# Kernel tuning notes

Hardware: AMD Instinct MI355X
Metric: run time of the kernel (lower is better)

## Reference

```python
import jax, jax.numpy as jnp
import numpy as np
import math

N = 32768
NUM_BATCH = 64
DIM_QK = 128
DIM_V = 256
M_FEATURES = 256
EPS_PHI = 1e-4
EPS_NORM = 1e-8


def _make_omega(nrows, ncols, rng):
    """Block-orthogonal random feature matrix, faithful to Attention._omega.
    Returns [ncols, nrows] (i.e. [dim_qk, m])."""
    nblocks = nrows // ncols
    blocks = []
    for _ in range(nblocks):
        q, _ = np.linalg.qr(rng.normal(size=(ncols, ncols)))
        blocks.append(q.T)
    missing = nrows - nblocks * ncols
    if missing > 0:
        q, _ = np.linalg.qr(rng.normal(size=(ncols, ncols)))
        blocks.append(q.T[:missing])
    norm = np.linalg.norm(rng.normal(size=(nrows, ncols)), axis=1, keepdims=True)
    return (norm * np.vstack(blocks)).T.astype(np.float32)


def setup_inputs() -> dict:
    key = jax.random.key(0)
    kq, kk, kv = jax.random.split(key, 3)
    Q = jax.random.normal(kq, (N, DIM_QK), dtype=jnp.float32)
    K = jax.random.normal(kk, (N, DIM_QK), dtype=jnp.float32)
    V = jax.random.normal(kv, (N, DIM_V), dtype=jnp.float32)
    # contiguous equal-size segments (64 molecules x 512 atoms)
    batch_seg = jnp.repeat(jnp.arange(NUM_BATCH, dtype=jnp.int32), N // NUM_BATCH)
    omega = jnp.asarray(_make_omega(M_FEATURES, DIM_QK, np.random.default_rng(0)))
    return {"Q": Q, "K": K, "V": V, "omega": omega,
            "num_batch": NUM_BATCH, "batch_seg": batch_seg}


def reference(Q, K, V, omega, num_batch, batch_seg):
    d = Q.shape[-1]
    m = omega.shape[-1]
    inv_sqrt_m = 1.0 / math.sqrt(m)

    def phi(X, is_query):
        U = (X / d ** 0.25) @ omega                       # [N, m]
        h = jnp.sum(X * X, axis=-1, keepdims=True) / (2.0 * d ** 0.5)
        if is_query:
            mx = jnp.max(U, axis=-1, keepdims=True)       # per-row max
        else:
            # per-segment max over all rows & features, gathered back per row
            seg_max = jax.ops.segment_max(jnp.max(U, axis=-1), batch_seg,
                                          num_segments=num_batch)
            mx = seg_max[batch_seg][:, None]
        return (jnp.exp(U - h - mx) + EPS_PHI) * inv_sqrt_m

    Qp = phi(Q, True)    # [N, m]
    Kp = phi(K, False)   # [N, m]

    # normalizer: Qp . (sum of Kp within segment)
    Ksum = jax.ops.segment_sum(Kp, batch_seg, num_segments=num_batch)  # [B, m]
    norm = jnp.sum(Qp * Ksum[batch_seg], axis=-1, keepdims=True) + EPS_NORM

    # Linear-attention equivalent of (mask * (Kp @ Qp^T))^T @ V:
    # out[i] = Qp[i] @ sum_{j in seg(i)} Kp[j] V[j]^T. Segments are
    # contiguous & equal-sized, so segment reductions become batched einsums.
    n_per = Q.shape[0] // num_batch
    Kpb = Kp.reshape(num_batch, n_per, m)
    Vb = V.reshape(num_batch, n_per, -1)
    KV = jnp.einsum('bnm,bnv->bmv', Kpb, Vb)              # [B, m, dv]
    Qpb = Qp.reshape(num_batch, n_per, m)
    out = jnp.einsum('bnm,bmv->bnv', Qpb, KV).reshape(Q.shape[0], -1)
    return out / norm
```

## Files before the change

### kernel.cpp

```cpp
#include <hip/hip_runtime.h>
#include <math.h>

#define NTOT 32768
#define NB   64
#define NPB  512
#define DQK  128
#define MF   256
#define DVV  256

#define QK_SCALE   0.29730177875068026f
#define INV_SQRT_M 0.0625f
#define EPS_PHI    1e-4f
#define EPS_NORM   1e-8f
#define EPS_ISM    (EPS_PHI * INV_SQRT_M)

typedef float f32x4  __attribute__((ext_vector_type(4)));
typedef short bf16x8 __attribute__((ext_vector_type(8)));
typedef unsigned short us4 __attribute__((ext_vector_type(4)));
typedef unsigned short us8 __attribute__((ext_vector_type(8)));

static __device__ __forceinline__ float red_max32(float v) {
    v = fmaxf(v, __shfl_xor(v, 1, 64));
    v = fmaxf(v, __shfl_xor(v, 2, 64));
    v = fmaxf(v, __shfl_xor(v, 4, 64));
    v = fmaxf(v, __shfl_xor(v, 8, 64));
    v = fmaxf(v, __shfl_xor(v, 16, 64));
    return v;
}
static __device__ __forceinline__ float red_sum16(float v) {
    v += __shfl_xor(v, 1, 64);
    v += __shfl_xor(v, 2, 64);
    v += __shfl_xor(v, 4, 64);
    v += __shfl_xor(v, 8, 64);
    return v;
}
static __device__ __forceinline__ float red_max16(float v) {
    v = fmaxf(v, __shfl_xor(v, 1, 64));
    v = fmaxf(v, __shfl_xor(v, 2, 64));
    v = fmaxf(v, __shfl_xor(v, 4, 64));
    v = fmaxf(v, __shfl_xor(v, 8, 64));
    return v;
}

static __device__ __forceinline__ void bfsplit(float x, unsigned short& h, unsigned short& l) {
    unsigned u = __float_as_uint(x);
    unsigned r = (u + 0x7fffu + ((u >> 16) & 1u)) & 0xffff0000u;
    h = (unsigned short)(r >> 16);
    float lo = x - __uint_as_float(r);
    unsigned v = __float_as_uint(lo);
    l = (unsigned short)((v + 0x7fffu + ((v >> 16) & 1u)) >> 16);
}

__global__ __launch_bounds__(256) void omsplit_kernel(
    const float* __restrict__ omega,
    unsigned short* __restrict__ OmFh, unsigned short* __restrict__ OmFl)
{
    const int k = blockIdx.x;
    const int m = threadIdx.x;
    unsigned short h, l;
    bfsplit(omega[k * MF + m], h, l);
    const int M16 = m >> 4, fr = m & 15;
    const int c = k >> 5, kk = k & 31;
    const int lane = fr + 16 * (kk >> 3);
    const size_t idx = ((size_t)(M16 * 4 + c) * 64 + lane) * 8 + (kk & 7);
    OmFh[idx] = h;
    OmFl[idx] = l;
}

template <bool IS_QUERY>
__global__ __launch_bounds__(256) void phi_kernel(
    const float* __restrict__ X,
    const unsigned short* __restrict__ OmFh, const unsigned short* __restrict__ OmFl,
    const float* __restrict__ Ksum,
    float* __restrict__ outF,
    unsigned short* __restrict__ outH, unsigned short* __restrict__ outL,
    float* __restrict__ aux)
{
    __shared__ __align__(16) float Xf[64][132];
    __shared__ float hS[64];
    __shared__ float mxW[4][64];
    __shared__ float npW[4][64];
    __shared__ float KsS[256];

    const int tid  = threadIdx.x;
    const int lane = tid & 63;
    const int w    = tid >> 6;
    const int fr   = lane & 15;
    const int k8   = (lane >> 4) * 8;
    const int rg   = (lane >> 4) * 4;
    const int row0 = blockIdx.x * 64;

    if (IS_QUERY) KsS[tid] = Ksum[(row0 >> 9) * MF + tid];

    float hp[8];
    {
        const float4* Xv = (const float4*)(X + (size_t)row0 * DQK);
        #pragma unroll
        for (int j = 0; j < 8; ++j) {
            int idx = tid + 256 * j;
            int r = idx >> 5, c4 = idx & 31;
            float4 v = Xv[idx];
            v.x *= QK_SCALE; v.y *= QK_SCALE; v.z *= QK_SCALE; v.w *= QK_SCALE;
            *(float4*)&Xf[r][c4 * 4] = v;
            hp[j] = v.x * v.x + v.y * v.y + v.z * v.z + v.w * v.w;
        }
    }
    __syncthreads();
    #pragma unroll
    for (int j = 0; j < 8; ++j) {
        hp[j] += __shfl_xor(hp[j], 1, 64);
        hp[j] += __shfl_xor(hp[j], 2, 64);
        hp[j] += __shfl_xor(hp[j], 4, 64);
        hp[j] += __shfl_xor(hp[j], 8, 64);
        hp[j] += __shfl_xor(hp[j], 16, 64);
    }
    if ((tid & 31) == 0) {
        #pragma unroll
        for (int j = 0; j < 8; ++j) hS[(tid >> 5) + 8 * j] = hp[j];
    }

    f32x4 acc[4][4] = {};
    #pragma unroll
    for (int c = 0; c < 4; ++c) {
        bf16x8 ah[4], al[4];
        #pragma unroll
        for (int t = 0; t < 4; ++t) {
            float a[8];
            *(float4*)&a[0] = *(const float4*)&Xf[t * 16 + fr][c * 32 + k8];
            *(float4*)&a[4] = *(const float4*)&Xf[t * 16 + fr][c * 32 + k8 + 4];
            unsigned short hh[8], ll[8];
            #pragma unroll
            for (int s = 0; s < 8; ++s) bfsplit(a[s], hh[s], ll[s]);
            ah[t] = *(bf16x8*)&hh[0];
            al[t] = *(bf16x8*)&ll[0];
        }
        #pragma unroll
        for (int u = 0; u < 4; ++u) {
            const size_t ob = ((size_t)((w * 4 + u) * 4 + c) * 64 + lane) * 8;
            bf16x8 bh = *(const bf16x8*)&OmFh[ob];
            bf16x8 bl = *(const bf16x8*)&OmFl[ob];
            #pragma unroll
            for (int t = 0; t < 4; ++t) {
                acc[t][u] = __builtin_amdgcn_mfma_f32_16x16x32_bf16(ah[t], bh, acc[t][u], 0, 0, 0);
                acc[t][u] = __builtin_amdgcn_mfma_f32_16x16x32_bf16(ah[t], bl, acc[t][u], 0, 0, 0);
                acc[t][u] = __builtin_amdgcn_mfma_f32_16x16x32_bf16(al[t], bh, acc[t][u], 0, 0, 0);
            }
        }
    }

    #pragma unroll
    for (int t = 0; t < 4; ++t) {
        #pragma unroll
        for (int g = 0; g < 4; ++g) {
            float m0 = fmaxf(fmaxf(acc[t][0][g], acc[t][1][g]),
                             fmaxf(acc[t][2][g], acc[t][3][g]));
            m0 = red_max16(m0);
            if (fr == 0) mxW[w][t * 16 + rg + g] = m0;
        }
    }
    __syncthreads();

    #pragma unroll
    for (int t = 0; t < 4; ++t) {
        #pragma unroll
        for (int g = 0; g < 4; ++g) {
            const int row  = t * 16 + rg + g;
            const int grow = row0 + row;
            const float mxa = fmaxf(fmaxf(mxW[0][row], mxW[1][row]),
                                    fmaxf(mxW[2][row], mxW[3][row]));
            const float hm = 0.5f * hS[row] + mxa;
            if (IS_QUERY) {
                float np = 0.f;
                #pragma unroll
                for (int u = 0; u < 4; ++u) {
                    const int col = w * 64 + u * 16 + fr;
                    const float q = (__expf(acc[t][u][g] - hm) + EPS_PHI) * INV_SQRT_M;
                    unsigned short qh, ql;
                    bfsplit(q, qh, ql);
                    outH[(size_t)grow * MF + col] = qh;
                    outL[(size_t)grow * MF + col] = ql;
                    np = fmaf(q, KsS[col], np);
                }
                np = red_sum16(np);
                if (fr == 0) npW[w][row] = np;
            } else {
                #pragma unroll
                for (int u = 0; u < 4; ++u)
                    outF[(size_t)grow * MF + w * 64 + u * 16 + fr] = __expf(acc[t][u][g] - hm);
                if (w == 0 && fr == 0) aux[grow] = mxa;
            }
        }
    }
    if (IS_QUERY) {
        __syncthreads();
        if (w == 0 && fr == 0) {
            #pragma unroll
            for (int t = 0; t < 4; ++t)
                #pragma unroll
                for (int g = 0; g < 4; ++g) {
                    const int row = t * 16 + rg + g;
                    aux[row0 + row] = npW[0][row] + npW[1][row] + npW[2][row] + npW[3][row];
                }
        }
    }
}

__global__ __launch_bounds__(256) void segsexp_kernel(
    const float* __restrict__ rmax, float* __restrict__ sexp)
{
    const int b = blockIdx.x, tid = threadIdx.x;
    const float r0 = rmax[b * NPB + tid];
    const float r1 = rmax[b * NPB + 256 + tid];
    float v = fmaxf(r0, r1);
    v = red_max32(v);
    v = fmaxf(v, __shfl_xor(v, 32, 64));
    __shared__ float red[4];
    if ((tid & 63) == 0) red[tid >> 6] = v;
    __syncthreads();
    const float smax = fmaxf(fmaxf(red[0], red[1]), fmaxf(red[2], red[3]));
    sexp[b * NPB + tid]       = __expf(r0 - smax);
    sexp[b * NPB + 256 + tid] = __expf(r1 - smax);
}

__global__ __launch_bounds__(256) void kv_kernel(
    const float* __restrict__ A, const float* __restrict__ V,
    const float* __restrict__ sexp,
    float* __restrict__ KV, float* __restrict__ P1,
    float* __restrict__ Ksum, float* __restrict__ KsumP)
{
    __shared__ __align__(16) float Af[32][132];
    __shared__ __align__(16) float Vf[32][132];
    __shared__ __align__(16) unsigned short KpH[128][40];
    __shared__ __align__(16) unsigned short KpL[128][40];
    __shared__ __align__(16) unsigned short VH[128][40];
    __shared__ __align__(16) unsigned short VL[128][40];

    const int tid  = threadIdx.x;
    const int lane = tid & 63;
    const int w    = tid >> 6;
    const int wr   = w >> 1;
    const int wc   = w & 1;
    const int fr   = lane & 15;
    const int k8   = (lane >> 4) * 8;
    const int rg   = (lane >> 4) * 4;

    const int vt = blockIdx.x, mt = blockIdx.y;
    const int b  = blockIdx.z >> 1, ch = blockIdx.z & 1;
    const int m0 = mt * 128, v0 = vt * 128;
    const size_t n0 = (size_t)b * NPB + ch * 256;

    const int ln  = tid >> 5;
    const int lm4 = tid & 31;
    const int tv  = tid >> 1;
    const int th  = tid & 1;

    f32x4 acc[4][4] = {};
    float4 ks4 = {0.f, 0.f, 0.f, 0.f};

    for (int c = 0; c < 8; ++c) {
        __syncthreads();
        #pragma unroll
        for (int j = 0; j < 4; ++j) {
            const size_t n = n0 + c * 32 + ln + 8 * j;
            float4 a  = *(const float4*)&A[n * MF + m0 + lm4 * 4];
            float4 vv = *(const float4*)&V[n * DVV + v0 + lm4 * 4];
            const float s2 = sexp[n] * INV_SQRT_M;
            float4 e;
            e.x = fmaf(a.x, s2, EPS_ISM);
            e.y = fmaf(a.y, s2, EPS_ISM);
            e.z = fmaf(a.z, s2, EPS_ISM);
            e.w = fmaf(a.w, s2, EPS_ISM);
            ks4.x += e.x; ks4.y += e.y; ks4.z += e.z; ks4.w += e.w;
            *(float4*)&Af[ln + 8 * j][lm4 * 4] = e;
            *(float4*)&Vf[ln + 8 * j][lm4 * 4] = vv;
        }
        __syncthreads();
        {
            unsigned short hh[16], ll[16];
            #pragma unroll
            for (int s = 0; s < 16; ++s)
                bfsplit(Af[th * 16 + s][tv], hh[s], ll[s]);
            *(us8*)&KpH[tv][th * 16]     = *(us8*)&hh[0];
            *(us8*)&KpH[tv][th * 16 + 8] = *(us8*)&hh[8];
            *(us8*)&KpL[tv][th * 16]     = *(us8*)&ll[0];
            *(us8*)&KpL[tv][th * 16 + 8] = *(us8*)&ll[8];
            #pragma unroll
            for (int s = 0; s < 16; ++s)
                bfsplit(Vf[th * 16 + s][tv], hh[s], ll[s]);
            *(us8*)&VH[tv][th * 16]     = *(us8*)&hh[0];
            *(us8*)&VH[tv][th * 16 + 8] = *(us8*)&hh[8];
            *(us8*)&VL[tv][th * 16]     = *(us8*)&ll[0];
            *(us8*)&VL[tv][th * 16 + 8] = *(us8*)&ll[8];
        }
        __syncthreads();
        bf16x8 ah[4], al[4];
        #pragma unroll
        for (int t = 0; t < 4; ++t) {
            ah[t] = *(const bf16x8*)&KpH[wr * 64 + t * 16 + fr][k8];
            al[t] = *(const bf16x8*)&KpL[wr * 64 + t * 16 + fr][k8];
        }
        #pragma unroll
        for (int u = 0; u < 4; ++u) {
            bf16x8 bh = *(const bf16x8*)&VH[wc * 64 + u * 16 + fr][k8];
            bf16x8 bl = *(const bf16x8*)&VL[wc * 64 + u * 16 + fr][k8];
            #pragma unroll
            for (int t = 0; t < 4; ++t) {
                acc[t][u] = __builtin_amdgcn_mfma_f32_16x16x32_bf16(ah[t], bh, acc[t][u], 0, 0, 0);
                acc[t][u] = __builtin_amdgcn_mfma_f32_16x16x32_bf16(ah[t], bl, acc[t][u], 0, 0, 0);
                acc[t][u] = __builtin_amdgcn_mfma_f32_16x16x32_bf16(al[t], bh, acc[t][u], 0, 0, 0);
            }
        }
    }

    float* __restrict__ dKV = ch ? P1 : KV;
    #pragma unroll
    for (int t = 0; t < 4; ++t) {
        #pragma unroll
        for (int g = 0; g < 4; ++g) {
            const int row = wr * 64 + t * 16 + rg + g;
            const size_t base = ((size_t)b * MF + m0 + row) * DVV + v0 + wc * 64;
            #pragma unroll
            for (int u = 0; u < 4; ++u)
                dKV[base + u * 16 + fr] = acc[t][u][g];
        }
    }

    if (vt == 0) {
        __syncthreads();
        float* scr = &Af[0][0];
        *(float4*)&scr[(ln * 32 + lm4) * 4] = ks4;
        __syncthreads();
        if (tid < 128) {
            float s = 0.f;
            #pragma unroll
            for (int g = 0; g < 8; ++g) s += scr[g * 128 + tid];
            (ch ? KsumP : Ksum)[b * MF + m0 + tid] = s;
        }
    }
}

__global__ __launch_bounds__(256) void kvreduce_kernel(
    float* __restrict__ KV, const float* __restrict__ P1,
    float* __restrict__ Ksum, const float* __restrict__ KsumP)
{
    const int idx = blockIdx.x * 256 + threadIdx.x;
    const int stride = gridDim.x * 256;
    const int TOT4 = NB * MF * DVV / 4;
    for (int i = idx; i < TOT4; i += stride) {
        float4 a = ((const float4*)KV)[i];
        float4 p = ((const float4*)P1)[i];
        a.x += p.x; a.y += p.y; a.z += p.z; a.w += p.w;
        ((float4*)KV)[i] = a;
    }
    const int KS4 = NB * MF / 4;
    for (int i = idx; i < KS4; i += stride) {
        float4 a = ((const float4*)Ksum)[i];
        float4 p = ((const float4*)KsumP)[i];
        a.x += p.x; a.y += p.y; a.z += p.z; a.w += p.w;
        ((float4*)Ksum)[i] = a;
    }
}

__global__ __launch_bounds__(256) void out_kernel(
    const unsigned short* __restrict__ QpH, const unsigned short* __restrict__ QpL,
    const float* __restrict__ KVm,
    const float* __restrict__ normv, float* __restrict__ out)
{
    __shared__ __align__(16) unsigned short Qh[128][40];
    __shared__ __align__(16) unsigned short Ql[128][40];
    __shared__ __align__(16) unsigned short Kh[128][40];
    __shared__ __align__(16) unsigned short Kl[128][40];
    __shared__ __align__(16) float Kf[32][132];
    __shared__ float nrmS[128];

    const int tid  = threadIdx.x;
    const int lane = tid & 63;
    const int w    = tid >> 6;
    const int wr   = w >> 1;
    const int wc   = w & 1;
    const int fr   = lane & 15;
    const int k8   = (lane >> 4) * 8;

    const int vt = blockIdx.x, rt = blockIdx.y, b = blockIdx.z;
    const int v0 = vt * 128;
    const int r0 = b * NPB + rt * 128;

    if (tid < 128) nrmS[tid] = normv[r0 + tid];

    const int qr  = tid >> 3;
    const int qm4 = tid & 7;
    const int km  = tid >> 5;
    const int kv4 = tid & 31;
    const int tv  = tid >> 1;
    const int th  = tid & 1;

    f32x4 acc[4][4] = {};

    for (int c = 0; c < 8; ++c) {
        const int mc = c * 32;
        __syncthreads();
        #pragma unroll
        for (int j = 0; j < 4; ++j) {
            const size_t qb = (size_t)(r0 + qr + 32 * j) * MF + mc + qm4 * 4;
            *(us4*)&Qh[qr + 32 * j][qm4 * 4] = *(const us4*)&QpH[qb];
            *(us4*)&Ql[qr + 32 * j][qm4 * 4] = *(const us4*)&QpL[qb];
            *(float4*)&Kf[km + 8 * j][kv4 * 4] =
                *(const float4*)&KVm[((size_t)b * MF + mc + km + 8 * j) * DVV + v0 + kv4 * 4];
        }
        __syncthreads();
        {
            unsigned short hh[16], ll[16];
            #pragma unroll
            for (int s = 0; s < 16; ++s)
                bfsplit(Kf[th * 16 + s][tv], hh[s], ll[s]);
            *(us8*)&Kh[tv][th * 16]     = *(us8*)&hh[0];
            *(us8*)&Kh[tv][th * 16 + 8] = *(us8*)&hh[8];
            *(us8*)&Kl[tv][th * 16]     = *(us8*)&ll[0];
            *(us8*)&Kl[tv][th * 16 + 8] = *(us8*)&ll[8];
        }
        __syncthreads();
        bf16x8 ah[4], al[4];
        #pragma unroll
        for (int t = 0; t < 4; ++t) {
            ah[t] = *(const bf16x8*)&Qh[wr * 64 + t * 16 + fr][k8];
            al[t] = *(const bf16x8*)&Ql[wr * 64 + t * 16 + fr][k8];
        }
        #pragma unroll
        for (int u = 0; u < 4; ++u) {
            bf16x8 bh = *(const bf16x8*)&Kh[wc * 64 + u * 16 + fr][k8];
            bf16x8 bl = *(const bf16x8*)&Kl[wc * 64 + u * 16 + fr][k8];
            #pragma unroll
            for (int t = 0; t < 4; ++t) {
                acc[t][u] = __builtin_amdgcn_mfma_f32_16x16x32_bf16(ah[t], bh, acc[t][u], 0, 0, 0);
                acc[t][u] = __builtin_amdgcn_mfma_f32_16x16x32_bf16(ah[t], bl, acc[t][u], 0, 0, 0);
                acc[t][u] = __builtin_amdgcn_mfma_f32_16x16x32_bf16(al[t], bh, acc[t][u], 0, 0, 0);
            }
        }
    }

    const int rg = (lane >> 4) * 4;
    #pragma unroll
    for (int t = 0; t < 4; ++t) {
        #pragma unroll
        for (int g = 0; g < 4; ++g) {
            const int row = wr * 64 + t * 16 + rg + g;
            const float inv = 1.0f / (nrmS[row] + EPS_NORM);
            const size_t base = (size_t)(r0 + row) * DVV + v0 + wc * 64;
            #pragma unroll
            for (int u = 0; u < 4; ++u)
                out[base + u * 16 + fr] = acc[t][u][g] * inv;
        }
    }
}

extern "C" void kernel_launch(void* const* d_in, const int* in_sizes, int n_in,
                              void* d_out, int out_size, void* d_ws, size_t ws_size,
                              hipStream_t stream)
{
    const float* Q     = (const float*)d_in[0];
    const float* K     = (const float*)d_in[1];
    const float* V     = (const float*)d_in[2];
    const float* omega = (const float*)d_in[3];
    float* out = (float*)d_out;

    float* ws    = (float*)d_ws;
    float* Qp    = ws;
    float* A     = Qp    + (size_t)NTOT * MF;
    float* KV    = A     + (size_t)NTOT * MF;
    float* Ksum  = KV    + (size_t)NB * MF * DVV;
    float* KsumP = Ksum  + (size_t)NB * MF;
    float* rmaxA = KsumP + (size_t)NB * MF;
    float* sexp  = rmaxA + NTOT;
    float* normv = sexp  + NTOT;
    unsigned short* OmFh = (unsigned short*)(normv + NTOT);
    unsigned short* OmFl = OmFh + (size_t)MF * DQK;

    float* P1 = Qp;
    unsigned short* QpH = (unsigned short*)Qp;
    unsigned short* QpL = QpH + (size_t)NTOT * MF;

    omsplit_kernel<<<DQK, 256, 0, stream>>>(omega, OmFh, OmFl);
    phi_kernel<false><<<NTOT / 64, 256, 0, stream>>>(K, OmFh, OmFl, (const float*)nullptr,
                                                     A, (unsigned short*)nullptr, (unsigned short*)nullptr, rmaxA);
    segsexp_kernel<<<NB, 256, 0, stream>>>(rmaxA, sexp);
    kv_kernel<<<dim3(2, 2, NB * 2), 256, 0, stream>>>(A, V, sexp, KV, P1, Ksum, KsumP);
    kvreduce_kernel<<<2048, 256, 0, stream>>>(KV, P1, Ksum, KsumP);
    phi_kernel<true ><<<NTOT / 64, 256, 0, stream>>>(Q, OmFh, OmFl, Ksum,
                                                     (float*)nullptr, QpH, QpL, normv);
    out_kernel<<<dim3(2, 4, NB), 256, 0, stream>>>(QpH, QpL, KV, normv, out);
}
```

Before: 211.2 us.

## Pre-split KV into bf16 hi/lo MFMA fragment layout in reduce kernel

The partial-sum reduce kernel now also splits KV into bf16 high/low halves and writes them in the per-lane MFMA B-fragment order. out_kernel then loads B fragments straight from global memory instead of staging fp32 KV in LDS and splitting it on every row tile. The out tile shrinks to 64 rows, doubling the grid, and the fp32 KV buffer is no longer read by out_kernel. This removes redundant bf16 splitting, two barriers and LDS traffic per chunk, at the cost of an extra write of the split buffers and uncoalesced-by-LDS global fragment reads that rely on the cache.

Result: slower. 220.9 us (+4.6%).

```diff
diff --git a/kernel.cpp b/kernel.cpp
--- a/kernel.cpp
+++ b/kernel.cpp
@@ -339,39 +339,56 @@
     }
 }
 
-__global__ __launch_bounds__(256) void kvreduce_kernel(
-    float* __restrict__ KV, const float* __restrict__ P1,
+__global__ __launch_bounds__(256) void kvsplit_kernel(
+    const float* __restrict__ KV, const float* __restrict__ P1,
+    unsigned short* __restrict__ KVFh, unsigned short* __restrict__ KVFl,
     float* __restrict__ Ksum, const float* __restrict__ KsumP)
 {
-    const int idx = blockIdx.x * 256 + threadIdx.x;
-    const int stride = gridDim.x * 256;
-    const int TOT4 = NB * MF * DVV / 4;
-    for (int i = idx; i < TOT4; i += stride) {
-        float4 a = ((const float4*)KV)[i];
-        float4 p = ((const float4*)P1)[i];
-        a.x += p.x; a.y += p.y; a.z += p.z; a.w += p.w;
-        ((float4*)KV)[i] = a;
-    }
-    const int KS4 = NB * MF / 4;
-    for (int i = idx; i < KS4; i += stride) {
-        float4 a = ((const float4*)Ksum)[i];
-        float4 p = ((const float4*)KsumP)[i];
-        a.x += p.x; a.y += p.y; a.z += p.z; a.w += p.w;
-        ((float4*)Ksum)[i] = a;
+    __shared__ __align__(16) float T[256][20];
+
+    const int V16 = blockIdx.x;
+    const int b   = blockIdx.y;
+    const int tid = threadIdx.x;
+
+    {
+        const size_t base = ((size_t)b * MF + tid) * DVV + V16 * 16;
+        #pragma unroll
+        for (int q = 0; q < 4; ++q) {
+            float4 a = *(const float4*)&KV[base + q * 4];
+            float4 p = *(const float4*)&P1[base + q * 4];
+            a.x += p.x; a.y += p.y; a.z += p.z; a.w += p.w;
+            *(float4*)&T[tid][q * 4] = a;
+        }
+    }
+    if (V16 == 0)
+        Ksum[b * MF + tid] += KsumP[b * MF + tid];
+    __syncthreads();
+
+    const int l  = tid & 63;
+    const int fr = l & 15;
+    const int s  = l >> 4;
+    const int c0 = tid >> 6;
+    #pragma unroll
+    for (int cc = 0; cc < 2; ++cc) {
+        const int c = c0 + cc * 4;
+        unsigned short hh[8], ll[8];
+        #pragma unroll
+        for (int e = 0; e < 8; ++e)
+            bfsplit(T[c * 32 + s * 8 + e][fr], hh[e], ll[e]);
+        const size_t idx = ((((size_t)b * 16 + V16) * 8 + c) * 64 + l) * 8;
+        *(us8*)&KVFh[idx] = *(us8*)&hh[0];
+        *(us8*)&KVFl[idx] = *(us8*)&ll[0];
     }
 }
 
 __global__ __launch_bounds__(256) void out_kernel(
     const unsigned short* __restrict__ QpH, const unsigned short* __restrict__ QpL,
-    const float* __restrict__ KVm,
+    const unsigned short* __restrict__ KVFh, const unsigned short* __restrict__ KVFl,
     const float* __restrict__ normv, float* __restrict__ out)
 {
-    __shared__ __align__(16) unsigned short Qh[128][40];
-    __shared__ __align__(16) unsigned short Ql[128][40];
-    __shared__ __align__(16) unsigned short Kh[128][40];
-    __shared__ __align__(16) unsigned short Kl[128][40];
-    __shared__ __align__(16) float Kf[32][132];
-    __shared__ float nrmS[128];
+    __shared__ __align__(16) unsigned short Qh[64][40];
+    __shared__ __align__(16) unsigned short Ql[64][40];
+    __shared__ float nrmS[64];
 
     const int tid  = threadIdx.x;
     const int lane = tid & 63;
@@ -383,54 +400,38 @@
 
     const int vt = blockIdx.x, rt = blockIdx.y, b = blockIdx.z;
     const int v0 = vt * 128;
-    const int r0 = b * NPB + rt * 128;
-
-    if (tid < 128) nrmS[tid] = normv[r0 + tid];
+    const int r0 = b * NPB + rt * 64;
+
+    if (tid < 64) nrmS[tid] = normv[r0 + tid];
 
     const int qr  = tid >> 3;
     const int qm4 = tid & 7;
-    const int km  = tid >> 5;
-    const int kv4 = tid & 31;
-    const int tv  = tid >> 1;
-    const int th  = tid & 1;
-
-    f32x4 acc[4][4] = {};
+
+    f32x4 acc[2][4] = {};
 
     for (int c = 0; c < 8; ++c) {
         const int mc = c * 32;
         __syncthreads();
         #pragma unroll
-        for (int j = 0; j < 4; ++j) {
+        for (int j = 0; j < 2; ++j) {
             const size_t qb = (size_t)(r0 + qr + 32 * j) * MF + mc + qm4 * 4;
             *(us4*)&Qh[qr + 32 * j][qm4 * 4] = *(const us4*)&QpH[qb];
             *(us4*)&Ql[qr + 32 * j][qm4 * 4] = *(const us4*)&QpL[qb];
-            *(float4*)&Kf[km + 8 * j][kv4 * 4] =
-                *(const float4*)&KVm[((size_t)b * MF + mc + km + 8 * j) * DVV + v0 + kv4 * 4];
-        }
-        __syncthreads();
-        {
-            unsigned short hh[16], ll[16];
-            #pragma unroll
-            for (int s = 0; s < 16; ++s)
-                bfsplit(Kf[th * 16 + s][tv], hh[s], ll[s]);
-            *(us8*)&Kh[tv][th * 16]     = *(us8*)&hh[0];
-            *(us8*)&Kh[tv][th * 16 + 8] = *(us8*)&hh[8];
-            *(us8*)&Kl[tv][th * 16]     = *(us8*)&ll[0];
-            *(us8*)&Kl[tv][th * 16 + 8] = *(us8*)&ll[8];
-        }
-        __syncthreads();
-        bf16x8 ah[4], al[4];
-        #pragma unroll
-        for (int t = 0; t < 4; ++t) {
-            ah[t] = *(const bf16x8*)&Qh[wr * 64 + t * 16 + fr][k8];
-            al[t] = *(const bf16x8*)&Ql[wr * 64 + t * 16 + fr][k8];
+        }
+        __syncthreads();
+        bf16x8 ah[2], al[2];
+        #pragma unroll
+        for (int t = 0; t < 2; ++t) {
+            ah[t] = *(const bf16x8*)&Qh[wr * 32 + t * 16 + fr][k8];
+            al[t] = *(const bf16x8*)&Ql[wr * 32 + t * 16 + fr][k8];
         }
         #pragma unroll
         for (int u = 0; u < 4; ++u) {
-            bf16x8 bh = *(const bf16x8*)&Kh[wc * 64 + u * 16 + fr][k8];
-            bf16x8 bl = *(const bf16x8*)&Kl[wc * 64 + u * 16 + fr][k8];
-            #pragma unroll
-            for (int t = 0; t < 4; ++t) {
+            const size_t kb = ((((size_t)b * 16 + vt * 8 + wc * 4 + u) * 8 + c) * 64 + lane) * 8;
+            bf16x8 bh = *(const bf16x8*)&KVFh[kb];
+            bf16x8 bl = *(const bf16x8*)&KVFl[kb];
+            #pragma unroll
+            for (int t = 0; t < 2; ++t) {
                 acc[t][u] = __builtin_amdgcn_mfma_f32_16x16x32_bf16(ah[t], bh, acc[t][u], 0, 0, 0);
                 acc[t][u] = __builtin_amdgcn_mfma_f32_16x16x32_bf16(ah[t], bl, acc[t][u], 0, 0, 0);
                 acc[t][u] = __builtin_amdgcn_mfma_f32_16x16x32_bf16(al[t], bh, acc[t][u], 0, 0, 0);
@@ -440,10 +441,10 @@
 
     const int rg = (lane >> 4) * 4;
     #pragma unroll
-    for (int t = 0; t < 4; ++t) {
+    for (int t = 0; t < 2; ++t) {
         #pragma unroll
         for (int g = 0; g < 4; ++g) {
-            const int row = wr * 64 + t * 16 + rg + g;
+            const int row = wr * 32 + t * 16 + rg + g;
             const float inv = 1.0f / (nrmS[row] + EPS_NORM);
             const size_t base = (size_t)(r0 + row) * DVV + v0 + wc * 64;
             #pragma unroll
@@ -478,14 +479,16 @@
     float* P1 = Qp;
     unsigned short* QpH = (unsigned short*)Qp;
     unsigned short* QpL = QpH + (size_t)NTOT * MF;
+    unsigned short* KVFh = (unsigned short*)A;
+    unsigned short* KVFl = KVFh + (size_t)NB * MF * DVV;
 
     omsplit_kernel<<<DQK, 256, 0, stream>>>(omega, OmFh, OmFl);
     phi_kernel<false><<<NTOT / 64, 256, 0, stream>>>(K, OmFh, OmFl, (const float*)nullptr,
                                                      A, (unsigned short*)nullptr, (unsigned short*)nullptr, rmaxA);
     segsexp_kernel<<<NB, 256, 0, stream>>>(rmaxA, sexp);
     kv_kernel<<<dim3(2, 2, NB * 2), 256, 0, stream>>>(A, V, sexp, KV, P1, Ksum, KsumP);
-    kvreduce_kernel<<<2048, 256, 0, stream>>>(KV, P1, Ksum, KsumP);
+    kvsplit_kernel<<<dim3(16, NB), 256, 0, stream>>>(KV, P1, KVFh, KVFl, Ksum, KsumP);
     phi_kernel<true ><<<NTOT / 64, 256, 0, stream>>>(Q, OmFh, OmFl, Ksum,
                                                      (float*)nullptr, QpH, QpL, normv);
-    out_kernel<<<dim3(2, 4, NB), 256, 0, stream>>>(QpH, QpL, KV, normv, out);
-}
+    out_kernel<<<dim3(2, 8, NB), 256, 0, stream>>>(QpH, QpL, KVFh, KVFl, normv, out);
+}
```
